# Kernel tuning notes

Hardware: AMD Instinct MI355X
Metric: run time of the kernel (lower is better)

Reference implementation:

```python
import jax, jax.numpy as jnp
import numpy as np

B, D_IN, H, A, L, HEADS, C = 1024, 512, 768, 5001, 4, 2, 2
N_DATA = 56000.0
NEG = -1e30


def _gru_step(x, h, Wih, Whh, bih, bhh):
    # torch nn.GRU gate order: r, z, n
    gi = x @ Wih + bih            # [B, 3H]
    gh = h @ Whh + bhh            # [B, 3H]
    i_r, i_z, i_n = jnp.split(gi, 3, axis=-1)
    h_r, h_z, h_n = jnp.split(gh, 3, axis=-1)
    r = jax.nn.sigmoid(i_r + h_r)
    z = jax.nn.sigmoid(i_z + h_z)
    n = jnp.tanh(i_n + r * h_n)
    return (1.0 - z) * n + z * h


def _atom_selector(cls, mask, Wih, Whh, bih, bhh, hW, hb, ae_w, key):
    # cls: [B, H]; mask: [B, A] int32 (mutable copy); dropout in eval mode (identity)
    h = jnp.zeros_like(cls)
    cur_in = cls
    ae_const = jax.lax.stop_gradient(ae_w)
    probs = []
    max_index = None
    rows = jnp.arange(B)
    for j in range(L):
        h = _gru_step(cur_in, h, Wih, Whh, bih, bhh)
        logits = h @ hW + hb                      # [B, A]
        if j == 0:
            col0 = jnp.where(mask.sum(axis=-1) == 0, 1, mask[:, 0])
            mask = mask.at[:, 0].set(col0)
        else:
            mask = jnp.where((max_index == 0)[:, None], 0, mask)
            mask = mask.at[:, 0].set(1)
        masked = jnp.where(mask > 0, logits, NEG)
        u = jax.random.uniform(jax.random.fold_in(key, j), (B, A), minval=1e-9, maxval=1.0)
        g = -jnp.log(-jnp.log(u))
        y_soft = jax.nn.softmax(masked + g, axis=-1)  # tau = 1
        ind = jnp.argmax(y_soft, axis=-1)             # [B]
        y_hard = jax.nn.one_hot(ind, A, dtype=y_soft.dtype)
        prob = y_hard + y_soft - jax.lax.stop_gradient(y_soft)  # straight-through
        mask = mask.at[rows, ind].set(0)              # scatter-zero chosen atoms
        probs.append(prob)
        max_index = ind
        cur_in = cls + prob @ ae_const                # atom embedding feedback
    return jnp.stack(probs, axis=1)                   # [B, L, A]


def reference(x, x_mask, W1, b1, W2, b2, W3, b3, gru_Wih, gru_Whh, gru_bih, gru_bhh,
              head_W, head_b, ae_w, ce_Wmu, ce_bmu, ce_Wcov, ce_bcov, alpha):
    # linear_base MLP
    h = jax.nn.relu(x @ W1 + b1)
    h = jax.nn.relu(h @ W2 + b2)
    h = h @ W3 + b3                                   # cls embedding [B, H]
    key = jax.random.key(42)
    atom_probs, cps = [], []
    for i in range(HEADS):
        ap = _atom_selector(h, x_mask, gru_Wih[i], gru_Whh[i], gru_bih[i], gru_bhh[i],
                            head_W[i], head_b[i], ae_w, jax.random.fold_in(key, i))
        atom_probs.append(ap)
        # consequent estimator stand-in: mu [B,C], coverage [B]
        pooled = ap.mean(axis=1)                      # [B, A]
        mu = jax.nn.sigmoid(pooled @ ce_Wmu + ce_bmu)
        coverage = jax.nn.sigmoid(pooled @ ce_Wcov + ce_bcov)
        n = coverage * N_DATA
        sf = (alpha[0] / n)[:, None]                  # [B, 1] -> broadcast to [B, C]
        cp = (mu + sf) / (1.0 + 2.0 * sf)
        cps.append(cp)
    mat_cp = jnp.stack(cps, axis=1)                   # [B, HEADS, C]
    out = jnp.log(mat_cp.mean(axis=1))                # [B, C]
    return out, jnp.stack(atom_probs, axis=1), mat_cp


def setup_inputs() -> dict:
    key = jax.random.key(0)
    ks = jax.random.split(key, 16)
    s = 0.02
    nrm = lambda k, sh: jax.random.normal(k, sh, dtype=jnp.float32) * s
    return {
        'x': jax.random.normal(ks[0], (B, D_IN), dtype=jnp.float32),
        'x_mask': jax.random.randint(ks[1], (B, A), 0, 2, dtype=jnp.int32),
        'W1': nrm(ks[2], (D_IN, H)), 'b1': jnp.zeros((H,), jnp.float32),
        'W2': nrm(ks[3], (H, H)), 'b2': jnp.zeros((H,), jnp.float32),
        'W3': nrm(ks[4], (H, H)), 'b3': jnp.zeros((H,), jnp.float32),
        'gru_Wih': nrm(ks[5], (HEADS, H, 3 * H)), 'gru_Whh': nrm(ks[6], (HEADS, H, 3 * H)),
        'gru_bih': jnp.zeros((HEADS, 3 * H), jnp.float32), 'gru_bhh': jnp.zeros((HEADS, 3 * H), jnp.float32),
        'head_W': nrm(ks[7], (HEADS, H, A)), 'head_b': jnp.zeros((HEADS, A), jnp.float32),
        'ae_w': nrm(ks[8], (A, H)),
        'ce_Wmu': nrm(ks[9], (A, C)), 'ce_bmu': jnp.zeros((C,), jnp.float32),
        'ce_Wcov': nrm(ks[10], (A,)), 'ce_bcov': jnp.zeros((), jnp.float32),
        'alpha': jnp.ones((1,), jnp.float32),
    }
```

## Files before the change

kernel.cpp:

```cpp
#include <hip/hip_runtime.h>
#include <hip/hip_bf16.h>
#include <stdint.h>
#include <stddef.h>

#define B_DIM   1024
#define DIN     512
#define H_DIM   768
#define A_DIM   5001
#define NHEADS  2
#define NSTEPS  4
#define C_DIM   2
#define NEG_VAL -1e30f
#define BH      (B_DIM * H_DIM)

typedef unsigned short u16;
typedef __attribute__((ext_vector_type(8))) short v8s;
typedef __attribute__((ext_vector_type(4))) float v4f;

typedef const __attribute__((address_space(1))) uint32_t* gas_ptr;
typedef __attribute__((address_space(3))) uint32_t* las_ptr;

__device__ __forceinline__ void load_lds16(const void* g, void* l) {
  __builtin_amdgcn_global_load_lds((gas_ptr)g, (las_ptr)l, 16, 0, 0);
}

__host__ __device__ inline uint32_t rotl32(uint32_t x, int d) {
  return (x << d) | (x >> (32 - d));
}

__host__ __device__ inline void threefry2x32(uint32_t k0, uint32_t k1,
                                             uint32_t x0, uint32_t x1,
                                             uint32_t& o0, uint32_t& o1) {
  uint32_t ks2 = k0 ^ k1 ^ 0x1BD11BDAu;
  x0 += k0; x1 += k1;
#define TFR(d) { x0 += x1; x1 = rotl32(x1, (d)); x1 ^= x0; }
  TFR(13) TFR(15) TFR(26) TFR(6)  x0 += k1;  x1 += ks2 + 1u;
  TFR(17) TFR(29) TFR(16) TFR(24) x0 += ks2; x1 += k0 + 2u;
  TFR(13) TFR(15) TFR(26) TFR(6)  x0 += k0;  x1 += k1 + 3u;
  TFR(17) TFR(29) TFR(16) TFR(24) x0 += k1;  x1 += ks2 + 4u;
  TFR(13) TFR(15) TFR(26) TFR(6)  x0 += ks2; x1 += k0 + 5u;
#undef TFR
  o0 = x0; o1 = x1;
}

__device__ inline float gumbel_noise(uint32_t k0, uint32_t k1, uint32_t idx) {
  uint32_t o0, o1;
  threefry2x32(k0, k1, 0u, idx, o0, o1);
  uint32_t bits = o0 ^ o1;
  float f = __uint_as_float(0x3f800000u | (bits >> 9)) - 1.0f;
  float u = fmaxf(1e-9f, f * (1.0f - 1e-9f) + 1e-9f);
  return -logf(-logf(u));
}

__device__ inline float sigmoidf_(float x) { return 0.5f * tanhf(0.5f * x) + 0.5f; }

__device__ inline void split_bf16(float x, u16& hi, u16& lo) {
  __hip_bfloat16 h = __float2bfloat16(x);
  float hf = __bfloat162float(h);
  __hip_bfloat16 l = __float2bfloat16(x - hf);
  hi = *(const u16*)&h;
  lo = *(const u16*)&l;
}

__global__ __launch_bounds__(256) void gemm_bias_act(
    const float* __restrict__ A, const float* __restrict__ B,
    const float* __restrict__ bias, float* __restrict__ C,
    int M, int N, int K, int act) {
  __shared__ float As[16][65];
  __shared__ float Bs[16][64];
  int tid = threadIdx.x;
  int bm = blockIdx.y * 64, bn = blockIdx.x * 64;
  int tx = tid & 15, ty = tid >> 4;
  float acc[4][4] = {};
  for (int k0 = 0; k0 < K; k0 += 16) {
#pragma unroll
    for (int r = 0; r < 4; ++r) {
      int m = (tid >> 4) + r * 16;
      int k = tid & 15;
      As[k][m] = A[(size_t)(bm + m) * K + k0 + k];
    }
#pragma unroll
    for (int r = 0; r < 4; ++r) {
      int n = tid & 63;
      int k = (tid >> 6) + r * 4;
      int gn = bn + n;
      Bs[k][n] = (gn < N) ? B[(size_t)(k0 + k) * N + gn] : 0.0f;
    }
    __syncthreads();
#pragma unroll
    for (int kk = 0; kk < 16; ++kk) {
      float a[4], bb[4];
#pragma unroll
      for (int i = 0; i < 4; ++i) a[i] = As[kk][ty * 4 + i];
#pragma unroll
      for (int jj = 0; jj < 4; ++jj) bb[jj] = Bs[kk][tx * 4 + jj];
#pragma unroll
      for (int i = 0; i < 4; ++i)
#pragma unroll
        for (int jj = 0; jj < 4; ++jj) acc[i][jj] = fmaf(a[i], bb[jj], acc[i][jj]);
    }
    __syncthreads();
  }
#pragma unroll
  for (int i = 0; i < 4; ++i) {
    int m = bm + ty * 4 + i;
#pragma unroll
    for (int jj = 0; jj < 4; ++jj) {
      int n = bn + tx * 4 + jj;
      if (n < N) {
        float v = acc[i][jj] + bias[n];
        if (act == 1) v = fmaxf(v, 0.0f);
        C[(size_t)m * N + n] = v;
      }
    }
  }
}

__global__ __launch_bounds__(256) void transpose_split(
    const float* __restrict__ W, u16* __restrict__ hi, u16* __restrict__ lo,
    int K, int N, size_t inStride, size_t outStride) {
  const int e = blockIdx.z;
  const float* Win = W + (size_t)e * inStride;
  u16* ho = hi + (size_t)e * outStride;
  u16* loo = lo + (size_t)e * outStride;
  __shared__ float tile[32][33];
  const int k0 = blockIdx.y * 32, n0 = blockIdx.x * 32;
  const int tx = threadIdx.x & 31, ty = threadIdx.x >> 5;
#pragma unroll
  for (int r = ty; r < 32; r += 8) {
    int n = n0 + tx;
    tile[r][tx] = (n < N) ? Win[(size_t)(k0 + r) * N + n] : 0.0f;
  }
  __syncthreads();
#pragma unroll
  for (int r = ty; r < 32; r += 8) {
    int n = n0 + r, k = k0 + tx;
    if (n < N) {
      u16 h, l;
      split_bf16(tile[tx][r], h, l);
      ho[(size_t)n * K + k] = h;
      loo[(size_t)n * K + k] = l;
    }
  }
}

struct GemmS {
  const u16* Ah[4]; const u16* Al[4];
  const u16* Bh[4]; const u16* Bl[4];
  const float* bias[4]; float* C[4];
};

__global__ __launch_bounds__(256, 2) void gemm_mfma(
    GemmS gs, int K, int N, int Nclamp, long long ldc, int nbx, int nby) {
  const int e = blockIdx.y;
  const int nwg = nbx * nby;
  const int chunk = nwg >> 3;
  const int orig = blockIdx.x;
  const int lid = (orig & 7) * chunk + (orig >> 3);
  const int by = lid % nby;
  const int bx = lid / nby;
  const int bm = by * 128, bn = bx * 128;

  __shared__ __align__(16) u16 lds[4][128 * 32];

  const int tid = threadIdx.x;
  const int wv = tid >> 6, ln = tid & 63;
  const int wr = wv >> 1, wc = wv & 1;
  const int lk = ln >> 4;
  const int lm = ln & 15;
  const int fswz = (lm >> 1) & 3;

  const int lrow = ln >> 2;
  const int slot = (ln & 3) ^ ((lrow >> 1) & 3);
  const u16* tsrc = (wv == 0) ? gs.Ah[e] : (wv == 1) ? gs.Al[e]
                  : (wv == 2) ? gs.Bh[e] : gs.Bl[e];
  const int isB = (wv >= 2);
  const int rowbase = isB ? bn : bm;

  const float* bias = gs.bias[e];
  float* C = gs.C[e];

  v4f acc[4][4];
#pragma unroll
  for (int i = 0; i < 4; ++i)
#pragma unroll
    for (int j = 0; j < 4; ++j) acc[i][j] = (v4f){0.f, 0.f, 0.f, 0.f};

  for (int k0 = 0; k0 < K; k0 += 32) {
#pragma unroll
    for (int i = 0; i < 8; ++i) {
      int gr = rowbase + i * 16 + lrow;
      if (isB && gr >= Nclamp) gr = Nclamp - 1;
      const u16* gp = tsrc + (size_t)gr * K + k0 + slot * 8;
      load_lds16(gp, (void*)&lds[wv][i * 512]);
    }
    __syncthreads();

    v8s ah[4], al[4], bh[4], bl[4];
#pragma unroll
    for (int mi = 0; mi < 4; ++mi) {
      const int r = wr * 64 + mi * 16 + lm;
      const int off = r * 32 + ((lk ^ fswz) * 8);
      ah[mi] = *(const v8s*)&lds[0][off];
      al[mi] = *(const v8s*)&lds[1][off];
    }
#pragma unroll
    for (int ni = 0; ni < 4; ++ni) {
      const int r = wc * 64 + ni * 16 + lm;
      const int off = r * 32 + ((lk ^ fswz) * 8);
      bh[ni] = *(const v8s*)&lds[2][off];
      bl[ni] = *(const v8s*)&lds[3][off];
    }
#pragma unroll
    for (int mi = 0; mi < 4; ++mi)
#pragma unroll
      for (int ni = 0; ni < 4; ++ni)
        acc[mi][ni] = __builtin_amdgcn_mfma_f32_16x16x32_bf16(ah[mi], bh[ni], acc[mi][ni], 0, 0, 0);
#pragma unroll
    for (int mi = 0; mi < 4; ++mi)
#pragma unroll
      for (int ni = 0; ni < 4; ++ni)
        acc[mi][ni] = __builtin_amdgcn_mfma_f32_16x16x32_bf16(ah[mi], bl[ni], acc[mi][ni], 0, 0, 0);
#pragma unroll
    for (int mi = 0; mi < 4; ++mi)
#pragma unroll
      for (int ni = 0; ni < 4; ++ni)
        acc[mi][ni] = __builtin_amdgcn_mfma_f32_16x16x32_bf16(al[mi], bh[ni], acc[mi][ni], 0, 0, 0);

    __syncthreads();
  }

#pragma unroll
  for (int mi = 0; mi < 4; ++mi) {
    const int m = bm + wr * 64 + mi * 16 + lk * 4;
#pragma unroll
    for (int ni = 0; ni < 4; ++ni) {
      const int n = bn + wc * 64 + ni * 16 + lm;
      if (n < N) {
        const float bv = bias[n];
        float* cp = C + (size_t)m * ldc + n;
#pragma unroll
        for (int r = 0; r < 4; ++r)
          cp[(size_t)r * ldc] = acc[mi][ni][r] + bv;
      }
    }
  }
}

__global__ __launch_bounds__(256) void init_state_kernel(
    const float* __restrict__ cls, float* __restrict__ h2,
    u16* __restrict__ h_hi, u16* __restrict__ h_lo,
    u16* __restrict__ cur_hi, u16* __restrict__ cur_lo) {
  int idx = blockIdx.x * blockDim.x + threadIdx.x;
  if (idx >= 2 * BH) return;
  int rem = idx % BH;
  h2[idx] = 0.0f;
  h_hi[idx] = 0; h_lo[idx] = 0;
  u16 h, l;
  split_bf16(cls[rem], h, l);
  cur_hi[idx] = h; cur_lo[idx] = l;
}

__global__ __launch_bounds__(256) void gru_combine_kernel(
    const float* __restrict__ gi2, const float* __restrict__ gh2, float* __restrict__ h2,
    u16* __restrict__ h_hi, u16* __restrict__ h_lo) {
  int idx = blockIdx.x * blockDim.x + threadIdx.x;
  if (idx >= 2 * BH) return;
  int e = idx / BH, rem = idx % BH;
  int b = rem / H_DIM, c = rem - b * H_DIM;
  const float* gib = gi2 + ((size_t)e * B_DIM + b) * 3 * H_DIM;
  const float* ghb = gh2 + ((size_t)e * B_DIM + b) * 3 * H_DIM;
  float ir = gib[c], iz = gib[H_DIM + c], inn = gib[2 * H_DIM + c];
  float hr = ghb[c], hz = ghb[H_DIM + c], hn = ghb[2 * H_DIM + c];
  float r = sigmoidf_(ir + hr);
  float z = sigmoidf_(iz + hz);
  float n = tanhf(inn + r * hn);
  float hv = (1.0f - z) * n + z * h2[idx];
  h2[idx] = hv;
  u16 h, l;
  split_bf16(hv, h, l);
  h_hi[idx] = h; h_lo[idx] = l;
}

__global__ __launch_bounds__(256) void curin_kernel(
    const float* __restrict__ cls, const float* __restrict__ ae_w,
    const int* __restrict__ indb, int j,
    u16* __restrict__ cur_hi, u16* __restrict__ cur_lo) {
  int idx = blockIdx.x * blockDim.x + threadIdx.x;
  if (idx >= 2 * BH) return;
  int e = idx / BH, rem = idx % BH;
  int b = rem / H_DIM, c = rem - b * H_DIM;
  int ind = indb[(e * NSTEPS + j) * B_DIM + b];
  float v = cls[rem] + ae_w[(size_t)ind * H_DIM + c];
  u16 h, l;
  split_bf16(v, h, l);
  cur_hi[idx] = h; cur_lo[idx] = l;
}

#define STH 256
#define PER_TH 20

__global__ __launch_bounds__(STH) void sample_kernel(
    float* __restrict__ probs, const int* __restrict__ x_mask,
    int* __restrict__ indb, int j, uint4 keys) {
  int b = blockIdx.x;
  int e = blockIdx.y;
  int t = threadIdx.x;
  uint32_t k0 = (e == 0) ? keys.x : keys.z;
  uint32_t k1 = (e == 0) ? keys.y : keys.w;
  __shared__ float rv[STH];
  __shared__ int ri[STH];
  __shared__ int s_ind;

  float* prow = probs + (((size_t)b * NHEADS + e) * NSTEPS + j) * A_DIM;
  const int* mrow = x_mask + (size_t)b * A_DIM;

  int prev[3];
  bool dead = false;
  for (int tt = 0; tt < j; ++tt) {
    prev[tt] = indb[(e * NSTEPS + tt) * B_DIM + b];
    if (prev[tt] == 0) dead = true;
  }

  bool rowany = true;
  if (j == 0) {
    int any = 0;
    for (int a = t; a < A_DIM; a += STH) any |= mrow[a];
    ri[t] = any; __syncthreads();
    for (int s = STH / 2; s > 0; s >>= 1) {
      if (t < s) ri[t] |= ri[t + s];
      __syncthreads();
    }
    rowany = (ri[0] != 0);
    __syncthreads();
  }

  float v[PER_TH];
  float lmax = -3.0e38f;
#pragma unroll
  for (int s = 0; s < PER_TH; ++s) {
    int a = t + s * STH;
    float val = -3.0e38f;
    if (a < A_DIM) {
      int m;
      if (j == 0) {
        m = (a == 0) ? (rowany ? mrow[0] : 1) : mrow[a];
      } else if (a == 0) {
        m = 1;
      } else if (dead) {
        m = 0;
      } else {
        m = mrow[a];
        if (m) {
          for (int tt = 0; tt < j; ++tt)
            if (prev[tt] == a) { m = 0; break; }
        }
      }
      if (m > 0)
        val = prow[a] + gumbel_noise(k0, k1, (uint32_t)(b * A_DIM + a));
    }
    v[s] = val;
    lmax = fmaxf(lmax, val);
  }

  rv[t] = lmax; __syncthreads();
  for (int s = STH / 2; s > 0; s >>= 1) {
    if (t < s) rv[t] = fmaxf(rv[t], rv[t + s]);
    __syncthreads();
  }
  float m = rv[0]; __syncthreads();

  float lsum = 0.0f;
#pragma unroll
  for (int s = 0; s < PER_TH; ++s) {
    int a = t + s * STH;
    float ev = (a < A_DIM && v[s] > -1.0e37f) ? expf(v[s] - m) : 0.0f;
    v[s] = ev; lsum += ev;
  }
  rv[t] = lsum; __syncthreads();
  for (int s = STH / 2; s > 0; s >>= 1) {
    if (t < s) rv[t] += rv[t + s];
    __syncthreads();
  }
  float ssum = rv[0]; __syncthreads();

  float besty = -1.0f; int besti = A_DIM;
#pragma unroll
  for (int s = 0; s < PER_TH; ++s) {
    int a = t + s * STH;
    if (a < A_DIM) {
      float y = v[s] / ssum;
      if (y > besty) { besty = y; besti = a; }
    }
  }
  rv[t] = besty; ri[t] = besti; __syncthreads();
  for (int s = STH / 2; s > 0; s >>= 1) {
    if (t < s) {
      float y2 = rv[t + s]; int i2 = ri[t + s];
      if (y2 > rv[t] || (y2 == rv[t] && i2 < ri[t])) { rv[t] = y2; ri[t] = i2; }
    }
    __syncthreads();
  }
  if (t == 0) { s_ind = ri[0]; indb[(e * NSTEPS + j) * B_DIM + b] = ri[0]; }
  __syncthreads();
  int ind = s_ind;

  for (int a = t; a < A_DIM; a += STH) prow[a] = (a == ind) ? 1.0f : 0.0f;
}

__global__ __launch_bounds__(256) void head_final_kernel(
    const int* __restrict__ indb, const float* __restrict__ Wmu,
    const float* __restrict__ bmu, const float* __restrict__ Wcov,
    const float* __restrict__ bcov, const float* __restrict__ alpha,
    float* __restrict__ matcp) {
  int idx = blockIdx.x * blockDim.x + threadIdx.x;
  if (idx >= NHEADS * B_DIM) return;
  int e = idx / B_DIM, b = idx - e * B_DIM;
  float a0 = 0.0f, a1 = 0.0f, ac = 0.0f;
  for (int j = 0; j < NSTEPS; ++j) {
    int ind = indb[(e * NSTEPS + j) * B_DIM + b];
    a0 += 0.25f * Wmu[(size_t)ind * C_DIM + 0];
    a1 += 0.25f * Wmu[(size_t)ind * C_DIM + 1];
    ac += 0.25f * Wcov[ind];
  }
  float mu0 = sigmoidf_(a0 + bmu[0]);
  float mu1 = sigmoidf_(a1 + bmu[1]);
  float cov = sigmoidf_(ac + bcov[0]);
  float n = cov * 56000.0f;
  float sf = alpha[0] / n;
  float denom = 1.0f + 2.0f * sf;
  matcp[((size_t)b * NHEADS + e) * C_DIM + 0] = (mu0 + sf) / denom;
  matcp[((size_t)b * NHEADS + e) * C_DIM + 1] = (mu1 + sf) / denom;
}

__global__ __launch_bounds__(256) void final_out_kernel(
    const float* __restrict__ matcp, float* __restrict__ out) {
  int idx = blockIdx.x * blockDim.x + threadIdx.x;
  if (idx >= B_DIM * C_DIM) return;
  int b = idx / C_DIM, c = idx - b * C_DIM;
  float s = matcp[((size_t)b * NHEADS + 0) * C_DIM + c] +
            matcp[((size_t)b * NHEADS + 1) * C_DIM + c];
  out[idx] = logf(s * 0.5f);
}

extern "C" void kernel_launch(void* const* d_in, const int* in_sizes, int n_in,
                              void* d_out, int out_size, void* d_ws, size_t ws_size,
                              hipStream_t stream) {
  const float* x     = (const float*)d_in[0];
  const int*   xmask = (const int*)d_in[1];
  const float* W1 = (const float*)d_in[2];  const float* b1 = (const float*)d_in[3];
  const float* W2 = (const float*)d_in[4];  const float* b2 = (const float*)d_in[5];
  const float* W3 = (const float*)d_in[6];  const float* b3 = (const float*)d_in[7];
  const float* gWih = (const float*)d_in[8];  const float* gWhh = (const float*)d_in[9];
  const float* gbih = (const float*)d_in[10]; const float* gbhh = (const float*)d_in[11];
  const float* hW = (const float*)d_in[12];   const float* hb = (const float*)d_in[13];
  const float* ae_w = (const float*)d_in[14];
  const float* Wmu  = (const float*)d_in[15]; const float* bmu  = (const float*)d_in[16];
  const float* Wcov = (const float*)d_in[17]; const float* bcov = (const float*)d_in[18];
  const float* alpha = (const float*)d_in[19];

  float* out = (float*)d_out;
  float* probs = out + (size_t)B_DIM * C_DIM;
  float* matcp = probs + (size_t)B_DIM * NHEADS * NSTEPS * A_DIM;

  const int HG = 3 * H_DIM;
  uint8_t* wsp = (uint8_t*)d_ws;
  auto alloc = [&](size_t bytes) {
    uint8_t* p = wsp;
    wsp += (bytes + 255) & ~(size_t)255;
    return p;
  };
  float* cls  = (float*)alloc((size_t)BH * 4);
  float* h2   = (float*)alloc((size_t)2 * BH * 4);
  float* gi2  = (float*)alloc((size_t)2 * B_DIM * HG * 4);
  float* gh2  = (float*)alloc((size_t)2 * B_DIM * HG * 4);
  u16* h_hi   = (u16*)alloc((size_t)2 * BH * 2);
  u16* h_lo   = (u16*)alloc((size_t)2 * BH * 2);
  u16* cur_hi = (u16*)alloc((size_t)2 * BH * 2);
  u16* cur_lo = (u16*)alloc((size_t)2 * BH * 2);
  u16* WihT_h = (u16*)alloc((size_t)2 * HG * H_DIM * 2);
  u16* WihT_l = (u16*)alloc((size_t)2 * HG * H_DIM * 2);
  u16* WhhT_h = (u16*)alloc((size_t)2 * HG * H_DIM * 2);
  u16* WhhT_l = (u16*)alloc((size_t)2 * HG * H_DIM * 2);
  u16* hWT_h  = (u16*)alloc((size_t)2 * A_DIM * H_DIM * 2);
  u16* hWT_l  = (u16*)alloc((size_t)2 * A_DIM * H_DIM * 2);
  int* indb   = (int*)alloc((size_t)NHEADS * NSTEPS * B_DIM * 4);
  float* t1 = gi2;
  float* t2 = gh2;

  dim3 blk(256);

  transpose_split<<<dim3(HG / 32, H_DIM / 32, 2), blk, 0, stream>>>(
      gWih, WihT_h, WihT_l, H_DIM, HG, (size_t)H_DIM * HG, (size_t)HG * H_DIM);
  transpose_split<<<dim3(HG / 32, H_DIM / 32, 2), blk, 0, stream>>>(
      gWhh, WhhT_h, WhhT_l, H_DIM, HG, (size_t)H_DIM * HG, (size_t)HG * H_DIM);
  transpose_split<<<dim3((A_DIM + 31) / 32, H_DIM / 32, 2), blk, 0, stream>>>(
      hW, hWT_h, hWT_l, H_DIM, A_DIM, (size_t)H_DIM * A_DIM, (size_t)A_DIM * H_DIM);

  auto gemm64 = [&](const float* Am, const float* Bm, const float* bias, float* Cm,
                    int M, int N, int K, int act) {
    dim3 grid((N + 63) / 64, M / 64);
    gemm_bias_act<<<grid, blk, 0, stream>>>(Am, Bm, bias, Cm, M, N, K, act);
  };
  gemm64(x, W1, b1, t1, B_DIM, H_DIM, DIN, 1);
  gemm64(t1, W2, b2, t2, B_DIM, H_DIM, H_DIM, 1);
  gemm64(t2, W3, b3, cls, B_DIM, H_DIM, H_DIM, 0);

  init_state_kernel<<<(2 * BH + 255) / 256, blk, 0, stream>>>(cls, h2, h_hi, h_lo, cur_hi, cur_lo);

  uint32_t bk0 = 0u, bk1 = 42u;
  uint32_t hk[2][2];
  threefry2x32(bk0, bk1, 0u, 0u, hk[0][0], hk[0][1]);
  threefry2x32(bk0, bk1, 0u, 1u, hk[1][0], hk[1][1]);

  for (int j = 0; j < NSTEPS; ++j) {
    GemmS gb;
    for (int head = 0; head < NHEADS; ++head) {
      gb.Ah[head * 2 + 0] = cur_hi + (size_t)head * BH;
      gb.Al[head * 2 + 0] = cur_lo + (size_t)head * BH;
      gb.Bh[head * 2 + 0] = WihT_h + (size_t)head * HG * H_DIM;
      gb.Bl[head * 2 + 0] = WihT_l + (size_t)head * HG * H_DIM;
      gb.bias[head * 2 + 0] = gbih + (size_t)head * HG;
      gb.C[head * 2 + 0] = gi2 + (size_t)head * B_DIM * HG;
      gb.Ah[head * 2 + 1] = h_hi + (size_t)head * BH;
      gb.Al[head * 2 + 1] = h_lo + (size_t)head * BH;
      gb.Bh[head * 2 + 1] = WhhT_h + (size_t)head * HG * H_DIM;
      gb.Bl[head * 2 + 1] = WhhT_l + (size_t)head * HG * H_DIM;
      gb.bias[head * 2 + 1] = gbhh + (size_t)head * HG;
      gb.C[head * 2 + 1] = gh2 + (size_t)head * B_DIM * HG;
    }
    gemm_mfma<<<dim3((HG / 128) * (B_DIM / 128), 4), blk, 0, stream>>>(
        gb, H_DIM, HG, HG, (long long)HG, HG / 128, B_DIM / 128);

    gru_combine_kernel<<<(2 * BH + 255) / 256, blk, 0, stream>>>(gi2, gh2, h2, h_hi, h_lo);

    GemmS lb;
    for (int head = 0; head < NHEADS; ++head) {
      lb.Ah[head] = h_hi + (size_t)head * BH;
      lb.Al[head] = h_lo + (size_t)head * BH;
      lb.Bh[head] = hWT_h + (size_t)head * A_DIM * H_DIM;
      lb.Bl[head] = hWT_l + (size_t)head * A_DIM * H_DIM;
      lb.bias[head] = hb + (size_t)head * A_DIM;
      lb.C[head] = probs + (size_t)(head * NSTEPS + j) * A_DIM;
      lb.Ah[head + 2] = lb.Ah[head]; lb.Al[head + 2] = lb.Al[head];
      lb.Bh[head + 2] = lb.Bh[head]; lb.Bl[head + 2] = lb.Bl[head];
      lb.bias[head + 2] = lb.bias[head]; lb.C[head + 2] = lb.C[head];
    }
    gemm_mfma<<<dim3(40 * (B_DIM / 128), 2), blk, 0, stream>>>(
        lb, H_DIM, A_DIM, A_DIM, (long long)NHEADS * NSTEPS * A_DIM, 40, B_DIM / 128);

    uint32_t s00, s01, s10, s11;
    threefry2x32(hk[0][0], hk[0][1], 0u, (uint32_t)j, s00, s01);
    threefry2x32(hk[1][0], hk[1][1], 0u, (uint32_t)j, s10, s11);
    uint4 keys; keys.x = s00; keys.y = s01; keys.z = s10; keys.w = s11;
    sample_kernel<<<dim3(B_DIM, NHEADS), dim3(STH), 0, stream>>>(probs, xmask, indb, j, keys);

    if (j < NSTEPS - 1)
      curin_kernel<<<(2 * BH + 255) / 256, blk, 0, stream>>>(cls, ae_w, indb, j, cur_hi, cur_lo);
  }

  head_final_kernel<<<(NHEADS * B_DIM + 255) / 256, blk, 0, stream>>>(
      indb, Wmu, bmu, Wcov, bcov, alpha, matcp);
  final_out_kernel<<<(B_DIM * C_DIM + 255) / 256, blk, 0, stream>>>(matcp, out);
}
```

Before: 1.003 ms.

## Split-K the MLP GEMMs and skip the zero-state hidden GEMM on step zero

The three base MLP GEMMs now use a split-K SIMT kernel that writes per-chunk partial sums, followed by a separate reduce kernel that adds the bias and applies ReLU. This raises block-level parallelism for these small GEMMs (192 blocks before), at the cost of extra partial-buffer traffic. On the first GRU step the hidden state is zero, so the h@Whh GEMM is dropped and a dedicated combine kernel uses the Whh bias directly. The init kernel no longer zeroes the hidden buffers, which saves memory writes.

Result: faster. 832.7 us (-17.0%).

```diff
diff --git a/kernel.cpp b/kernel.cpp
--- a/kernel.cpp
+++ b/kernel.cpp
@@ -62,17 +62,19 @@
   lo = *(const u16*)&l;
 }
 
-__global__ __launch_bounds__(256) void gemm_bias_act(
+__global__ __launch_bounds__(256) void gemm_splitk(
     const float* __restrict__ A, const float* __restrict__ B,
-    const float* __restrict__ bias, float* __restrict__ C,
-    int M, int N, int K, int act) {
+    float* __restrict__ part, int M, int N, int K, int kchunk) {
   __shared__ float As[16][65];
   __shared__ float Bs[16][64];
   int tid = threadIdx.x;
   int bm = blockIdx.y * 64, bn = blockIdx.x * 64;
+  const int s = blockIdx.z;
+  const int kb = s * kchunk;
+  const int ke = (kb + kchunk < K) ? (kb + kchunk) : K;
   int tx = tid & 15, ty = tid >> 4;
   float acc[4][4] = {};
-  for (int k0 = 0; k0 < K; k0 += 16) {
+  for (int k0 = kb; k0 < ke; k0 += 16) {
 #pragma unroll
     for (int r = 0; r < 4; ++r) {
       int m = (tid >> 4) + r * 16;
@@ -101,19 +103,29 @@
     }
     __syncthreads();
   }
+  float* po = part + (size_t)s * M * N;
 #pragma unroll
   for (int i = 0; i < 4; ++i) {
     int m = bm + ty * 4 + i;
 #pragma unroll
     for (int jj = 0; jj < 4; ++jj) {
       int n = bn + tx * 4 + jj;
-      if (n < N) {
-        float v = acc[i][jj] + bias[n];
-        if (act == 1) v = fmaxf(v, 0.0f);
-        C[(size_t)m * N + n] = v;
-      }
-    }
-  }
+      if (n < N) po[(size_t)m * N + n] = acc[i][jj];
+    }
+  }
+}
+
+__global__ __launch_bounds__(256) void reduce_bias_act(
+    const float* __restrict__ part, const float* __restrict__ bias,
+    float* __restrict__ C, int M, int N, int S, int act) {
+  int idx = blockIdx.x * blockDim.x + threadIdx.x;
+  if (idx >= M * N) return;
+  int n = idx % N;
+  float v = 0.0f;
+  for (int s = 0; s < S; ++s) v += part[(size_t)s * M * N + idx];
+  v += bias[n];
+  if (act == 1) v = fmaxf(v, 0.0f);
+  C[idx] = v;
 }
 
 __global__ __launch_bounds__(256) void transpose_split(
@@ -248,17 +260,35 @@
 }
 
 __global__ __launch_bounds__(256) void init_state_kernel(
-    const float* __restrict__ cls, float* __restrict__ h2,
-    u16* __restrict__ h_hi, u16* __restrict__ h_lo,
+    const float* __restrict__ cls,
     u16* __restrict__ cur_hi, u16* __restrict__ cur_lo) {
   int idx = blockIdx.x * blockDim.x + threadIdx.x;
   if (idx >= 2 * BH) return;
   int rem = idx % BH;
-  h2[idx] = 0.0f;
-  h_hi[idx] = 0; h_lo[idx] = 0;
   u16 h, l;
   split_bf16(cls[rem], h, l);
   cur_hi[idx] = h; cur_lo[idx] = l;
+}
+
+__global__ __launch_bounds__(256) void gru_combine_first(
+    const float* __restrict__ gi2, const float* __restrict__ gbhh, float* __restrict__ h2,
+    u16* __restrict__ h_hi, u16* __restrict__ h_lo) {
+  int idx = blockIdx.x * blockDim.x + threadIdx.x;
+  if (idx >= 2 * BH) return;
+  int e = idx / BH, rem = idx % BH;
+  int b = rem / H_DIM, c = rem - b * H_DIM;
+  const float* gib = gi2 + ((size_t)e * B_DIM + b) * 3 * H_DIM;
+  const float* bb = gbhh + (size_t)e * 3 * H_DIM;
+  float ir = gib[c], iz = gib[H_DIM + c], inn = gib[2 * H_DIM + c];
+  float hr = bb[c], hz = bb[H_DIM + c], hn = bb[2 * H_DIM + c];
+  float r = sigmoidf_(ir + hr);
+  float z = sigmoidf_(iz + hz);
+  float n = tanhf(inn + r * hn);
+  float hv = (1.0f - z) * n + z * 0.0f;
+  h2[idx] = hv;
+  u16 h, l;
+  split_bf16(hv, h, l);
+  h_hi[idx] = h; h_lo[idx] = l;
 }
 
 __global__ __launch_bounds__(256) void gru_combine_kernel(
@@ -485,8 +515,9 @@
   u16* hWT_h  = (u16*)alloc((size_t)2 * A_DIM * H_DIM * 2);
   u16* hWT_l  = (u16*)alloc((size_t)2 * A_DIM * H_DIM * 2);
   int* indb   = (int*)alloc((size_t)NHEADS * NSTEPS * B_DIM * 4);
+  float* parts = gh2;
   float* t1 = gi2;
-  float* t2 = gh2;
+  float* t2 = gi2 + BH;
 
   dim3 blk(256);
 
@@ -497,16 +528,18 @@
   transpose_split<<<dim3((A_DIM + 31) / 32, H_DIM / 32, 2), blk, 0, stream>>>(
       hW, hWT_h, hWT_l, H_DIM, A_DIM, (size_t)H_DIM * A_DIM, (size_t)A_DIM * H_DIM);
 
-  auto gemm64 = [&](const float* Am, const float* Bm, const float* bias, float* Cm,
-                    int M, int N, int K, int act) {
-    dim3 grid((N + 63) / 64, M / 64);
-    gemm_bias_act<<<grid, blk, 0, stream>>>(Am, Bm, bias, Cm, M, N, K, act);
-  };
-  gemm64(x, W1, b1, t1, B_DIM, H_DIM, DIN, 1);
-  gemm64(t1, W2, b2, t2, B_DIM, H_DIM, H_DIM, 1);
-  gemm64(t2, W3, b3, cls, B_DIM, H_DIM, H_DIM, 0);
-
-  init_state_kernel<<<(2 * BH + 255) / 256, blk, 0, stream>>>(cls, h2, h_hi, h_lo, cur_hi, cur_lo);
+  const int MN = B_DIM * H_DIM;
+  gemm_splitk<<<dim3(H_DIM / 64, B_DIM / 64, 4), blk, 0, stream>>>(
+      x, W1, parts, B_DIM, H_DIM, DIN, 128);
+  reduce_bias_act<<<(MN + 255) / 256, blk, 0, stream>>>(parts, b1, t1, B_DIM, H_DIM, 4, 1);
+  gemm_splitk<<<dim3(H_DIM / 64, B_DIM / 64, 6), blk, 0, stream>>>(
+      t1, W2, parts, B_DIM, H_DIM, H_DIM, 128);
+  reduce_bias_act<<<(MN + 255) / 256, blk, 0, stream>>>(parts, b2, t2, B_DIM, H_DIM, 6, 1);
+  gemm_splitk<<<dim3(H_DIM / 64, B_DIM / 64, 6), blk, 0, stream>>>(
+      t2, W3, parts, B_DIM, H_DIM, H_DIM, 128);
+  reduce_bias_act<<<(MN + 255) / 256, blk, 0, stream>>>(parts, b3, cls, B_DIM, H_DIM, 6, 0);
+
+  init_state_kernel<<<(2 * BH + 255) / 256, blk, 0, stream>>>(cls, cur_hi, cur_lo);
 
   uint32_t bk0 = 0u, bk1 = 42u;
   uint32_t hk[2][2];
@@ -514,25 +547,42 @@
   threefry2x32(bk0, bk1, 0u, 1u, hk[1][0], hk[1][1]);
 
   for (int j = 0; j < NSTEPS; ++j) {
-    GemmS gb;
-    for (int head = 0; head < NHEADS; ++head) {
-      gb.Ah[head * 2 + 0] = cur_hi + (size_t)head * BH;
-      gb.Al[head * 2 + 0] = cur_lo + (size_t)head * BH;
-      gb.Bh[head * 2 + 0] = WihT_h + (size_t)head * HG * H_DIM;
-      gb.Bl[head * 2 + 0] = WihT_l + (size_t)head * HG * H_DIM;
-      gb.bias[head * 2 + 0] = gbih + (size_t)head * HG;
-      gb.C[head * 2 + 0] = gi2 + (size_t)head * B_DIM * HG;
-      gb.Ah[head * 2 + 1] = h_hi + (size_t)head * BH;
-      gb.Al[head * 2 + 1] = h_lo + (size_t)head * BH;
-      gb.Bh[head * 2 + 1] = WhhT_h + (size_t)head * HG * H_DIM;
-      gb.Bl[head * 2 + 1] = WhhT_l + (size_t)head * HG * H_DIM;
-      gb.bias[head * 2 + 1] = gbhh + (size_t)head * HG;
-      gb.C[head * 2 + 1] = gh2 + (size_t)head * B_DIM * HG;
-    }
-    gemm_mfma<<<dim3((HG / 128) * (B_DIM / 128), 4), blk, 0, stream>>>(
-        gb, H_DIM, HG, HG, (long long)HG, HG / 128, B_DIM / 128);
-
-    gru_combine_kernel<<<(2 * BH + 255) / 256, blk, 0, stream>>>(gi2, gh2, h2, h_hi, h_lo);
+    if (j == 0) {
+      GemmS gb;
+      for (int head = 0; head < NHEADS; ++head) {
+        gb.Ah[head] = cur_hi + (size_t)head * BH;
+        gb.Al[head] = cur_lo + (size_t)head * BH;
+        gb.Bh[head] = WihT_h + (size_t)head * HG * H_DIM;
+        gb.Bl[head] = WihT_l + (size_t)head * HG * H_DIM;
+        gb.bias[head] = gbih + (size_t)head * HG;
+        gb.C[head] = gi2 + (size_t)head * B_DIM * HG;
+        gb.Ah[head + 2] = gb.Ah[head]; gb.Al[head + 2] = gb.Al[head];
+        gb.Bh[head + 2] = gb.Bh[head]; gb.Bl[head + 2] = gb.Bl[head];
+        gb.bias[head + 2] = gb.bias[head]; gb.C[head + 2] = gb.C[head];
+      }
+      gemm_mfma<<<dim3((HG / 128) * (B_DIM / 128), 2), blk, 0, stream>>>(
+          gb, H_DIM, HG, HG, (long long)HG, HG / 128, B_DIM / 128);
+      gru_combine_first<<<(2 * BH + 255) / 256, blk, 0, stream>>>(gi2, gbhh, h2, h_hi, h_lo);
+    } else {
+      GemmS gb;
+      for (int head = 0; head < NHEADS; ++head) {
+        gb.Ah[head * 2 + 0] = cur_hi + (size_t)head * BH;
+        gb.Al[head * 2 + 0] = cur_lo + (size_t)head * BH;
+        gb.Bh[head * 2 + 0] = WihT_h + (size_t)head * HG * H_DIM;
+        gb.Bl[head * 2 + 0] = WihT_l + (size_t)head * HG * H_DIM;
+        gb.bias[head * 2 + 0] = gbih + (size_t)head * HG;
+        gb.C[head * 2 + 0] = gi2 + (size_t)head * B_DIM * HG;
+        gb.Ah[head * 2 + 1] = h_hi + (size_t)head * BH;
+        gb.Al[head * 2 + 1] = h_lo + (size_t)head * BH;
+        gb.Bh[head * 2 + 1] = WhhT_h + (size_t)head * HG * H_DIM;
+        gb.Bl[head * 2 + 1] = WhhT_l + (size_t)head * HG * H_DIM;
+        gb.bias[head * 2 + 1] = gbhh + (size_t)head * HG;
+        gb.C[head * 2 + 1] = gh2 + (size_t)head * B_DIM * HG;
+      }
+      gemm_mfma<<<dim3((HG / 128) * (B_DIM / 128), 4), blk, 0, stream>>>(
+          gb, H_DIM, HG, HG, (long long)HG, HG / 128, B_DIM / 128);
+      gru_combine_kernel<<<(2 * BH + 255) / 256, blk, 0, stream>>>(gi2, gh2, h2, h_hi, h_lo);
+    }
 
     GemmS lb;
     for (int head = 0; head < NHEADS; ++head) {
```
